# Kernel tuning notes

Hardware: AMD Instinct MI355X
Metric: run time of the kernel (lower is better)

## Reference

```python
import jax, jax.numpy as jnp
import numpy as np

R, B, N, I, O, NB = 8, 4, 1024, 64, 64, 4
EPS = 1e-7  # keras.backend.epsilon()


def setup_inputs() -> dict:
    key = jax.random.key(0)
    ks = jax.random.split(key, 6)
    features = jax.random.normal(ks[0], (B, N, I), jnp.float32)
    adj = jax.random.randint(ks[1], (R, B, N, N), 0, 2, jnp.int32)  # stacked A[i]
    weight = jax.random.normal(ks[2], (NB, I, O), jnp.float32) * 0.1  # basis weights
    Wo = jax.random.normal(ks[3], (I, O), jnp.float32) * 0.1          # self-loop weight
    w_cmp = jax.random.normal(ks[4], (R, NB), jnp.float32) * 0.1      # basis coefficients
    b = jax.random.normal(ks[5], (O,), jnp.float32) * 0.1             # bias
    return {"features": features, "adj": adj, "weight": weight, "Wo": Wo, "w_cmp": w_cmp, "b": b}


def reference(features, adj, weight, Wo, w_cmp, b):
    # basis decomposition: per-relation weight [R, I, O]
    w_full = jnp.einsum('rb,bio->rio', w_cmp, weight)
    adj_f = adj.astype(features.dtype)                      # [R, B, N, N]
    # per-relation transform: x_r = features @ W_r -> [R, B, N, O]
    x = jnp.einsum('bni,rio->rbno', features, w_full)
    # batch_dot(edges^T, x): agg[r,b,n] = sum_m edges[r,b,m,n] * x[r,b,m]
    agg = jnp.einsum('rbmn,rbmo->rbno', adj_f, x)
    # original normalizer: K.sum(edges, axis=2, keepdims=True) -> row sums over last axis
    deg = adj_f.sum(axis=-1, keepdims=True)                 # [R, B, N, 1]
    agg = agg / (deg + EPS)
    self_x = features @ Wo                                  # [B, N, O]
    # concatenate [x_0 | x_1 | ... | x_{R-1} | self] along features
    concat = jnp.concatenate(
        [agg.transpose(1, 2, 0, 3).reshape(B, N, R * O), self_x], axis=-1
    )                                                       # [B, N, (R+1)*O]
    # faithful to original: reshape (..., O, R+1) then sum last axis
    out = concat.reshape(-1, N, O, R + 1).sum(axis=-1)      # [B, N, O]
    out = out + b
    return jax.nn.relu(out)
```

## Files before the change

### kernel.cpp

```cpp
#include <hip/hip_runtime.h>
#include <hip/hip_bf16.h>


#define NN 1024
#define EPSK 1e-7f

typedef __bf16 bf16x8 __attribute__((ext_vector_type(8)));
typedef float f32x4 __attribute__((ext_vector_type(4)));

__device__ __forceinline__ unsigned short f2bf(float f) {
  union { float f; unsigned int u; } v; v.f = f;
  return (unsigned short)((v.u + 0x7FFFu + ((v.u >> 16) & 1u)) >> 16);
}

__global__ __launch_bounds__(256) void prep_kernel(
    const float* __restrict__ feat,
    const float* __restrict__ weight,
    const float* __restrict__ Wo,
    const float* __restrict__ wcmp,
    float* __restrict__ xf,
    float* __restrict__ selfP)
{
  __shared__ __align__(16) unsigned short featL[128 * 72];
  __shared__ __align__(16) float wTf[64 * 65];
  __shared__ __align__(16) unsigned short wfold[16 * 72];
  __shared__ __align__(16) float stg[128 * 8];

  const int bid = blockIdx.x;
  const int t = threadIdx.x;
  const bool isSelf = bid >= 256;
  int r, b, chunk;
  if (!isSelf) { r = bid >> 5; b = (bid >> 3) & 3; chunk = bid & 7; }
  else { const int s2 = bid - 256; b = s2 >> 3; chunk = s2 & 7; r = 8; }
  const int n0 = chunk << 7;

  const float* fsrc = feat + ((size_t)(b * NN + n0)) * 64;
  #pragma unroll
  for (int p = 0; p < 8; ++p) {
    const int idx = p * 256 + t;
    const int row = idx >> 4, c4 = idx & 15;
    const float4 v = *reinterpret_cast<const float4*>(fsrc + row * 64 + c4 * 4);
    ushort4 u;
    u.x = f2bf(v.x); u.y = f2bf(v.y); u.z = f2bf(v.z); u.w = f2bf(v.w);
    *reinterpret_cast<ushort4*>(&featL[row * 72 + c4 * 4]) = u;
  }

  if (!isSelf) {
    const float wc0 = wcmp[r * 4 + 0], wc1 = wcmp[r * 4 + 1];
    const float wc2 = wcmp[r * 4 + 2], wc3 = wcmp[r * 4 + 3];
    #pragma unroll
    for (int jj = 0; jj < 16; ++jj) {
      const int e = jj * 256 + t;
      const int i = e >> 6, c = e & 63;
      wTf[c * 65 + i] = wc0 * weight[i * 64 + c] + wc1 * weight[4096 + i * 64 + c] +
                        wc2 * weight[8192 + i * 64 + c] + wc3 * weight[12288 + i * 64 + c];
    }
  } else {
    #pragma unroll
    for (int jj = 0; jj < 16; ++jj) {
      const int e = jj * 256 + t;
      const int i = e >> 6, c = e & 63;
      wTf[c * 65 + i] = Wo[i * 64 + c];
    }
  }
  __syncthreads();

  #pragma unroll
  for (int jj = 0; jj < 4; ++jj) {
    const int e = jj * 256 + t;
    const int s = e >> 6, i = e & 63;
    float sum = 0.f;
    if (s < 8) {
      const int c0 = 9 * s - r;
      const int clo = c0 < 0 ? 0 : c0;
      const int chi = (c0 + 8 > 63) ? 63 : c0 + 8;
      for (int c = clo; c <= chi; ++c) sum += wTf[c * 65 + i];
    }
    wfold[s * 72 + i] = f2bf(sum);
  }
  __syncthreads();

  const int w = t >> 6, lane = t & 63;
  const int li = lane & 15, lg = lane >> 4;

  f32x4 acc0 = {0.f, 0.f, 0.f, 0.f}, acc1 = {0.f, 0.f, 0.f, 0.f};
  #pragma unroll
  for (int ks = 0; ks < 2; ++ks) {
    const int kof = ks * 32 + lg * 8;
    const bf16x8 af = __builtin_bit_cast(bf16x8,
        *reinterpret_cast<const uint4*>(&wfold[li * 72 + kof]));
    const bf16x8 b0 = __builtin_bit_cast(bf16x8,
        *reinterpret_cast<const uint4*>(&featL[((2 * w + 0) * 16 + li) * 72 + kof]));
    const bf16x8 b1 = __builtin_bit_cast(bf16x8,
        *reinterpret_cast<const uint4*>(&featL[((2 * w + 1) * 16 + li) * 72 + kof]));
    acc0 = __builtin_amdgcn_mfma_f32_16x16x32_bf16(af, b0, acc0, 0, 0, 0);
    acc1 = __builtin_amdgcn_mfma_f32_16x16x32_bf16(af, b1, acc1, 0, 0, 0);
  }

  if (lg < 2) {
    #pragma unroll
    for (int qq = 0; qq < 4; ++qq) {
      const int s = lg * 4 + qq;
      stg[((2 * w + 0) * 16 + li) * 8 + s] = acc0[qq];
      stg[((2 * w + 1) * 16 + li) * 8 + s] = acc1[qq];
    }
  }
  __syncthreads();
  {
    float* dstF = isSelf ? (selfP + ((size_t)(b * NN + n0)) * 8)
                         : (xf + ((size_t)((r * 4 + b) * NN + n0)) * 8);
    *reinterpret_cast<float4*>(dstF + t * 4) =
        *reinterpret_cast<const float4*>(&stg[t * 4]);
  }
}

#define BODY(PK, G, K, PF)                                                      \
  {                                                                             \
    const int4 cur_ = PK;                                                       \
    if (PF) {                                                                   \
      PK = *reinterpret_cast<const int4*>(asrc + ((((G) << 4) + (K) + 16) << 10)); \
    }                                                                           \
    const int ps_ = cur_.x + cur_.y + cur_.z + cur_.w;                          \
    pk |= ((unsigned int)ps_) << (8 * ((K) & 3));                               \
    const float a0_ = (float)cur_.x, a1_ = (float)cur_.y;                       \
    const float a2_ = (float)cur_.z, a3_ = (float)cur_.w;                       \
    const float4 xlo_ =                                                         \
        *reinterpret_cast<const float4*>(&xsL[(((G) << 4) + (K)) * 8]);         \
    const float4 xhi_ =                                                         \
        *reinterpret_cast<const float4*>(&xsL[(((G) << 4) + (K)) * 8 + 4]);     \
    const float xv_[8] = {xlo_.x, xlo_.y, xlo_.z, xlo_.w,                       \
                          xhi_.x, xhi_.y, xhi_.z, xhi_.w};                      \
    _Pragma("unroll")                                                           \
    for (int s_ = 0; s_ < 8; ++s_) {                                            \
      acc0[s_] = fmaf(a0_, xv_[s_], acc0[s_]);                                  \
      acc1[s_] = fmaf(a1_, xv_[s_], acc1[s_]);                                  \
      acc2[s_] = fmaf(a2_, xv_[s_], acc2[s_]);                                  \
      acc3[s_] = fmaf(a3_, xv_[s_], acc3[s_]);                                  \
    }                                                                           \
    if (((K) & 3) == 3) {                                                       \
      degL[((G) * 4 + ((K) >> 2)) * 260 + t] = pk;                              \
      pk = 0u;                                                                  \
    }                                                                           \
  }

#define GROUP(G, PF)                                                            \
  BODY(P0, G, 0, PF) BODY(P1, G, 1, PF) BODY(P2, G, 2, PF) BODY(P3, G, 3, PF)   \
  BODY(P4, G, 4, PF) BODY(P5, G, 5, PF) BODY(P6, G, 6, PF) BODY(P7, G, 7, PF)   \
  BODY(P8, G, 8, PF) BODY(P9, G, 9, PF) BODY(P10, G, 10, PF)                    \
  BODY(P11, G, 11, PF) BODY(P12, G, 12, PF) BODY(P13, G, 13, PF)                \
  BODY(P14, G, 14, PF) BODY(P15, G, 15, PF)

__global__ __launch_bounds__(256, 1) void agg_kernel(
    const int* __restrict__ adj,
    const float* __restrict__ xf,
    float* __restrict__ aggP,
    float* __restrict__ deg)
{
  __shared__ __align__(16) float xsL[128 * 8];
  __shared__ __align__(16) unsigned int degL[32 * 260];

  const int bid = blockIdx.x;
  const int rb = bid >> 3, mc = bid & 7;
  const int m0 = mc << 7;
  const int t = threadIdx.x;

  const int* asrc = adj + (((size_t)rb) << 20) + (((size_t)m0) << 10) + (t << 2);

  int4 P0  = *reinterpret_cast<const int4*>(asrc + (0 << 10));
  int4 P1  = *reinterpret_cast<const int4*>(asrc + (1 << 10));
  int4 P2  = *reinterpret_cast<const int4*>(asrc + (2 << 10));
  int4 P3  = *reinterpret_cast<const int4*>(asrc + (3 << 10));
  int4 P4  = *reinterpret_cast<const int4*>(asrc + (4 << 10));
  int4 P5  = *reinterpret_cast<const int4*>(asrc + (5 << 10));
  int4 P6  = *reinterpret_cast<const int4*>(asrc + (6 << 10));
  int4 P7  = *reinterpret_cast<const int4*>(asrc + (7 << 10));
  int4 P8  = *reinterpret_cast<const int4*>(asrc + (8 << 10));
  int4 P9  = *reinterpret_cast<const int4*>(asrc + (9 << 10));
  int4 P10 = *reinterpret_cast<const int4*>(asrc + (10 << 10));
  int4 P11 = *reinterpret_cast<const int4*>(asrc + (11 << 10));
  int4 P12 = *reinterpret_cast<const int4*>(asrc + (12 << 10));
  int4 P13 = *reinterpret_cast<const int4*>(asrc + (13 << 10));
  int4 P14 = *reinterpret_cast<const int4*>(asrc + (14 << 10));
  int4 P15 = *reinterpret_cast<const int4*>(asrc + (15 << 10));

  {
    const float* xs = xf + ((size_t)(rb * NN + m0)) * 8;
    *reinterpret_cast<float4*>(&xsL[t * 4]) =
        *reinterpret_cast<const float4*>(xs + t * 4);
  }

  float acc0[8], acc1[8], acc2[8], acc3[8];
  #pragma unroll
  for (int s = 0; s < 8; ++s) { acc0[s] = 0.f; acc1[s] = 0.f; acc2[s] = 0.f; acc3[s] = 0.f; }

  __syncthreads();

  unsigned int pk = 0u;
  for (int g = 0; g < 7; ++g) {
    GROUP(g, 1)
  }
  GROUP(7, 0)

  {
    float* dst = aggP + (((size_t)(mc * 32 + rb)) * NN + 4 * (size_t)t) * 8;
    *reinterpret_cast<float4*>(dst + 0)  = make_float4(acc0[0], acc0[1], acc0[2], acc0[3]);
    *reinterpret_cast<float4*>(dst + 4)  = make_float4(acc0[4], acc0[5], acc0[6], acc0[7]);
    *reinterpret_cast<float4*>(dst + 8)  = make_float4(acc1[0], acc1[1], acc1[2], acc1[3]);
    *reinterpret_cast<float4*>(dst + 12) = make_float4(acc1[4], acc1[5], acc1[6], acc1[7]);
    *reinterpret_cast<float4*>(dst + 16) = make_float4(acc2[0], acc2[1], acc2[2], acc2[3]);
    *reinterpret_cast<float4*>(dst + 20) = make_float4(acc2[4], acc2[5], acc2[6], acc2[7]);
    *reinterpret_cast<float4*>(dst + 24) = make_float4(acc3[0], acc3[1], acc3[2], acc3[3]);
    *reinterpret_cast<float4*>(dst + 28) = make_float4(acc3[4], acc3[5], acc3[6], acc3[7]);
  }

  __syncthreads();

  if (t < 128) {
    const unsigned int* src = &degL[(t >> 2) * 260];
    const int sh = 8 * (t & 3);
    int sum = 0;
    #pragma unroll
    for (int c4 = 0; c4 < 64; ++c4) {
      const uint4 v = *reinterpret_cast<const uint4*>(src + c4 * 4);
      sum += (int)((v.x >> sh) & 0xFFu) + (int)((v.y >> sh) & 0xFFu) +
             (int)((v.z >> sh) & 0xFFu) + (int)((v.w >> sh) & 0xFFu);
    }
    deg[rb * NN + m0 + t] = (float)sum;
  }
}

__global__ __launch_bounds__(256) void out_kernel(
    const float* __restrict__ aggP,
    const float* __restrict__ selfP,
    const float* __restrict__ deg,
    const float* __restrict__ bias, float* __restrict__ out)
{
  const int gid = blockIdx.x * 256 + threadIdx.x;
  const int o = gid & 63;
  const int n = (gid >> 6) & 1023;
  const int b = gid >> 16;

  const int r1 = (9 * o) >> 6;
  const int r2 = (9 * o + 8) >> 6;

  float acc = bias[o];
  #pragma unroll
  for (int pass = 0; pass < 2; ++pass) {
    const int r = pass ? r2 : r1;
    if (pass && r2 == r1) break;
    float v;
    if (r < 8) {
      const int s = o - 7 * r;
      const size_t base = (((size_t)(r * 4 + b)) * NN + n) * 8 + s;
      float sum = 0.f;
      #pragma unroll
      for (int c = 0; c < 8; ++c) sum += aggP[base + (size_t)c * 262144];
      v = sum / (deg[(r * 4 + b) * NN + n] + EPSK);
    } else {
      v = selfP[((size_t)(b * NN + n)) * 8 + (o - 56)];
    }
    acc += v;
  }
  out[gid] = fmaxf(acc, 0.0f);
}

extern "C" void kernel_launch(void* const* d_in, const int* in_sizes, int n_in,
                              void* d_out, int out_size, void* d_ws, size_t ws_size,
                              hipStream_t stream) {
  const float* feat   = (const float*)d_in[0];
  const int*   adj    = (const int*)d_in[1];
  const float* weight = (const float*)d_in[2];
  const float* Wo     = (const float*)d_in[3];
  const float* wcmp   = (const float*)d_in[4];
  const float* bias   = (const float*)d_in[5];
  float* out = (float*)d_out;

  char* ws = (char*)d_ws;
  float* xf    = (float*)(ws);
  float* selfP = (float*)(ws + 1048576u);
  float* aggP  = (float*)(ws + 1048576u + 131072u);
  float* deg   = (float*)(ws + 1048576u + 131072u + 8388608u);

  prep_kernel<<<dim3(288), dim3(256), 0, stream>>>(feat, weight, Wo, wcmp, xf, selfP);
  agg_kernel<<<dim3(256), dim3(256), 0, stream>>>(adj, xf, aggP, deg);
  out_kernel<<<dim3(1024), dim3(256), 0, stream>>>(aggP, selfP, deg, bias, out);
}
```

Baseline: 38.42 us.

## Split aggregation across column quarters and reduce row partials in shared memory

Result: slower. 46.06 us (+19.9%).

```diff
diff --git a/kernel.cpp b/kernel.cpp
--- a/kernel.cpp
+++ b/kernel.cpp
@@ -19,7 +19,8 @@
     const float* __restrict__ Wo,
     const float* __restrict__ wcmp,
     float* __restrict__ xf,
-    float* __restrict__ selfP)
+    float* __restrict__ selfP,
+    float* __restrict__ deg)
 {
   __shared__ __align__(16) unsigned short featL[128 * 72];
   __shared__ __align__(16) float wTf[64 * 65];
@@ -33,6 +34,10 @@
   if (!isSelf) { r = bid >> 5; b = (bid >> 3) & 3; chunk = bid & 7; }
   else { const int s2 = bid - 256; b = s2 >> 3; chunk = s2 & 7; r = 8; }
   const int n0 = chunk << 7;
+
+  if (bid < 32) {
+    for (int k = t; k < NN; k += 256) deg[bid * NN + k] = 0.0f;
+  }
 
   const float* fsrc = feat + ((size_t)(b * NN + n0)) * 64;
   #pragma unroll
@@ -114,20 +119,19 @@
   }
 }
 
-#define BODY(PK, G, K, PF)                                                      \
+#define BODY(PK, I, K, PF)                                                      \
   {                                                                             \
     const int4 cur_ = PK;                                                       \
+    const int ml_ = 4 * (I) + tm;                                               \
     if (PF) {                                                                   \
-      PK = *reinterpret_cast<const int4*>(asrc + ((((G) << 4) + (K) + 16) << 10)); \
+      PK = *reinterpret_cast<const int4*>(asrc + ((size_t)(ml_ + 32) << 10));   \
     }                                                                           \
     const int ps_ = cur_.x + cur_.y + cur_.z + cur_.w;                          \
     pk |= ((unsigned int)ps_) << (8 * ((K) & 3));                               \
     const float a0_ = (float)cur_.x, a1_ = (float)cur_.y;                       \
     const float a2_ = (float)cur_.z, a3_ = (float)cur_.w;                       \
-    const float4 xlo_ =                                                         \
-        *reinterpret_cast<const float4*>(&xsL[(((G) << 4) + (K)) * 8]);         \
-    const float4 xhi_ =                                                         \
-        *reinterpret_cast<const float4*>(&xsL[(((G) << 4) + (K)) * 8 + 4]);     \
+    const float4 xlo_ = *reinterpret_cast<const float4*>(&xsL[ml_ * 8]);        \
+    const float4 xhi_ = *reinterpret_cast<const float4*>(&xsL[ml_ * 8 + 4]);    \
     const float xv_[8] = {xlo_.x, xlo_.y, xlo_.z, xlo_.w,                       \
                           xhi_.x, xhi_.y, xhi_.z, xhi_.w};                      \
     _Pragma("unroll")                                                           \
@@ -138,50 +142,33 @@
       acc3[s_] = fmaf(a3_, xv_[s_], acc3[s_]);                                  \
     }                                                                           \
     if (((K) & 3) == 3) {                                                       \
-      degL[((G) * 4 + ((K) >> 2)) * 260 + t] = pk;                              \
+      scratch4[(((I) >> 2) * 4 + tm) * 68 + tn] = pk;                           \
       pk = 0u;                                                                  \
     }                                                                           \
   }
 
 #define GROUP(G, PF)                                                            \
-  BODY(P0, G, 0, PF) BODY(P1, G, 1, PF) BODY(P2, G, 2, PF) BODY(P3, G, 3, PF)   \
-  BODY(P4, G, 4, PF) BODY(P5, G, 5, PF) BODY(P6, G, 6, PF) BODY(P7, G, 7, PF)   \
-  BODY(P8, G, 8, PF) BODY(P9, G, 9, PF) BODY(P10, G, 10, PF)                    \
-  BODY(P11, G, 11, PF) BODY(P12, G, 12, PF) BODY(P13, G, 13, PF)                \
-  BODY(P14, G, 14, PF) BODY(P15, G, 15, PF)
-
-__global__ __launch_bounds__(256, 1) void agg_kernel(
+  BODY(P0, 8 * (G) + 0, 0, PF) BODY(P1, 8 * (G) + 1, 1, PF)                     \
+  BODY(P2, 8 * (G) + 2, 2, PF) BODY(P3, 8 * (G) + 3, 3, PF)                     \
+  BODY(P4, 8 * (G) + 4, 4, PF) BODY(P5, 8 * (G) + 5, 5, PF)                     \
+  BODY(P6, 8 * (G) + 6, 6, PF) BODY(P7, 8 * (G) + 7, 7, PF)
+
+__global__ __launch_bounds__(256, 4) void agg_kernel(
     const int* __restrict__ adj,
     const float* __restrict__ xf,
     float* __restrict__ aggP,
     float* __restrict__ deg)
 {
   __shared__ __align__(16) float xsL[128 * 8];
-  __shared__ __align__(16) unsigned int degL[32 * 260];
+  __shared__ __align__(16) unsigned int scratch4[256 * 34];
 
   const int bid = blockIdx.x;
-  const int rb = bid >> 3, mc = bid & 7;
-  const int m0 = mc << 7;
+  const int rb = bid >> 5, mq = (bid >> 2) & 7, nq = bid & 3;
+  const int m0 = mq << 7, n0 = nq << 8;
   const int t = threadIdx.x;
-
-  const int* asrc = adj + (((size_t)rb) << 20) + (((size_t)m0) << 10) + (t << 2);
-
-  int4 P0  = *reinterpret_cast<const int4*>(asrc + (0 << 10));
-  int4 P1  = *reinterpret_cast<const int4*>(asrc + (1 << 10));
-  int4 P2  = *reinterpret_cast<const int4*>(asrc + (2 << 10));
-  int4 P3  = *reinterpret_cast<const int4*>(asrc + (3 << 10));
-  int4 P4  = *reinterpret_cast<const int4*>(asrc + (4 << 10));
-  int4 P5  = *reinterpret_cast<const int4*>(asrc + (5 << 10));
-  int4 P6  = *reinterpret_cast<const int4*>(asrc + (6 << 10));
-  int4 P7  = *reinterpret_cast<const int4*>(asrc + (7 << 10));
-  int4 P8  = *reinterpret_cast<const int4*>(asrc + (8 << 10));
-  int4 P9  = *reinterpret_cast<const int4*>(asrc + (9 << 10));
-  int4 P10 = *reinterpret_cast<const int4*>(asrc + (10 << 10));
-  int4 P11 = *reinterpret_cast<const int4*>(asrc + (11 << 10));
-  int4 P12 = *reinterpret_cast<const int4*>(asrc + (12 << 10));
-  int4 P13 = *reinterpret_cast<const int4*>(asrc + (13 << 10));
-  int4 P14 = *reinterpret_cast<const int4*>(asrc + (14 << 10));
-  int4 P15 = *reinterpret_cast<const int4*>(asrc + (15 << 10));
+  const int tm = t >> 6, tn = t & 63;
+
+  const int* asrc = adj + (((size_t)rb) << 20) + (((size_t)m0) << 10) + n0 + (tn << 2);
 
   {
     const float* xs = xf + ((size_t)(rb * NN + m0)) * 8;
@@ -189,6 +176,15 @@
         *reinterpret_cast<const float4*>(xs + t * 4);
   }
 
+  int4 P0 = *reinterpret_cast<const int4*>(asrc + ((size_t)(0 * 4 + tm) << 10));
+  int4 P1 = *reinterpret_cast<const int4*>(asrc + ((size_t)(1 * 4 + tm) << 10));
+  int4 P2 = *reinterpret_cast<const int4*>(asrc + ((size_t)(2 * 4 + tm) << 10));
+  int4 P3 = *reinterpret_cast<const int4*>(asrc + ((size_t)(3 * 4 + tm) << 10));
+  int4 P4 = *reinterpret_cast<const int4*>(asrc + ((size_t)(4 * 4 + tm) << 10));
+  int4 P5 = *reinterpret_cast<const int4*>(asrc + ((size_t)(5 * 4 + tm) << 10));
+  int4 P6 = *reinterpret_cast<const int4*>(asrc + ((size_t)(6 * 4 + tm) << 10));
+  int4 P7 = *reinterpret_cast<const int4*>(asrc + ((size_t)(7 * 4 + tm) << 10));
+
   float acc0[8], acc1[8], acc2[8], acc3[8];
   #pragma unroll
   for (int s = 0; s < 8; ++s) { acc0[s] = 0.f; acc1[s] = 0.f; acc2[s] = 0.f; acc3[s] = 0.f; }
@@ -196,36 +192,62 @@
   __syncthreads();
 
   unsigned int pk = 0u;
-  for (int g = 0; g < 7; ++g) {
+  for (int g = 0; g < 3; ++g) {
     GROUP(g, 1)
   }
-  GROUP(7, 0)
-
-  {
-    float* dst = aggP + (((size_t)(mc * 32 + rb)) * NN + 4 * (size_t)t) * 8;
-    *reinterpret_cast<float4*>(dst + 0)  = make_float4(acc0[0], acc0[1], acc0[2], acc0[3]);
-    *reinterpret_cast<float4*>(dst + 4)  = make_float4(acc0[4], acc0[5], acc0[6], acc0[7]);
-    *reinterpret_cast<float4*>(dst + 8)  = make_float4(acc1[0], acc1[1], acc1[2], acc1[3]);
-    *reinterpret_cast<float4*>(dst + 12) = make_float4(acc1[4], acc1[5], acc1[6], acc1[7]);
-    *reinterpret_cast<float4*>(dst + 16) = make_float4(acc2[0], acc2[1], acc2[2], acc2[3]);
-    *reinterpret_cast<float4*>(dst + 20) = make_float4(acc2[4], acc2[5], acc2[6], acc2[7]);
-    *reinterpret_cast<float4*>(dst + 24) = make_float4(acc3[0], acc3[1], acc3[2], acc3[3]);
-    *reinterpret_cast<float4*>(dst + 28) = make_float4(acc3[4], acc3[5], acc3[6], acc3[7]);
-  }
-
-  __syncthreads();
-
+  GROUP(3, 0)
+
+  __syncthreads();
+
+  float dsum = 0.f;
+  int mrow = 0;
   if (t < 128) {
-    const unsigned int* src = &degL[(t >> 2) * 260];
-    const int sh = 8 * (t & 3);
+    mrow = t;
+    const int k = mrow >> 4, j = (mrow >> 2) & 3, tmm = mrow & 3;
+    const unsigned int* src = &scratch4[(k * 4 + tmm) * 68];
+    const int sh = 8 * j;
     int sum = 0;
     #pragma unroll
-    for (int c4 = 0; c4 < 64; ++c4) {
+    for (int c4 = 0; c4 < 16; ++c4) {
       const uint4 v = *reinterpret_cast<const uint4*>(src + c4 * 4);
       sum += (int)((v.x >> sh) & 0xFFu) + (int)((v.y >> sh) & 0xFFu) +
              (int)((v.z >> sh) & 0xFFu) + (int)((v.w >> sh) & 0xFFu);
     }
-    deg[rb * NN + m0 + t] = (float)sum;
+    dsum = (float)sum;
+  }
+  __syncthreads();
+
+  float* accL = reinterpret_cast<float*>(scratch4);
+  #pragma unroll
+  for (int j = 0; j < 4; ++j) {
+    const float* a = (j == 0) ? acc0 : (j == 1) ? acc1 : (j == 2) ? acc2 : acc3;
+    *reinterpret_cast<float4*>(&accL[t * 34 + j * 8]) =
+        make_float4(a[0], a[1], a[2], a[3]);
+    *reinterpret_cast<float4*>(&accL[t * 34 + j * 8 + 4]) =
+        make_float4(a[4], a[5], a[6], a[7]);
+  }
+  if (t < 128) {
+    atomicAdd(&deg[rb * NN + m0 + mrow], dsum);
+  }
+  __syncthreads();
+
+  {
+    const int nl = t;
+    const int tn2 = nl >> 2, j2 = nl & 3;
+    float o8[8];
+    #pragma unroll
+    for (int s = 0; s < 8; ++s) o8[s] = 0.f;
+    #pragma unroll
+    for (int tm2 = 0; tm2 < 4; ++tm2) {
+      const int base = (tm2 * 64 + tn2) * 34 + j2 * 8;
+      const float4 lo = *reinterpret_cast<const float4*>(&accL[base]);
+      const float4 hi = *reinterpret_cast<const float4*>(&accL[base + 4]);
+      o8[0] += lo.x; o8[1] += lo.y; o8[2] += lo.z; o8[3] += lo.w;
+      o8[4] += hi.x; o8[5] += hi.y; o8[6] += hi.z; o8[7] += hi.w;
+    }
+    float* dst = aggP + ((size_t)((mq * 32 + rb) * NN + n0 + nl)) * 8;
+    *reinterpret_cast<float4*>(dst) = make_float4(o8[0], o8[1], o8[2], o8[3]);
+    *reinterpret_cast<float4*>(dst + 4) = make_float4(o8[4], o8[5], o8[6], o8[7]);
   }
 }
 
@@ -281,7 +303,7 @@
   float* aggP  = (float*)(ws + 1048576u + 131072u);
   float* deg   = (float*)(ws + 1048576u + 131072u + 8388608u);
 
-  prep_kernel<<<dim3(288), dim3(256), 0, stream>>>(feat, weight, Wo, wcmp, xf, selfP);
-  agg_kernel<<<dim3(256), dim3(256), 0, stream>>>(adj, xf, aggP, deg);
+  prep_kernel<<<dim3(288), dim3(256), 0, stream>>>(feat, weight, Wo, wcmp, xf, selfP, deg);
+  agg_kernel<<<dim3(1024), dim3(256), 0, stream>>>(adj, xf, aggP, deg);
   out_kernel<<<dim3(1024), dim3(256), 0, stream>>>(aggP, selfP, deg, bias, out);
 }
```
